# Optimization experiments

Hardware: AMD Instinct MI355X
Metric: run time of the kernel (lower is better)

## Reference

```python
import jax, jax.numpy as jnp
import numpy as np

N_NODES = 100000
N_EDGES = 600000
F_IN = 128
F_OUT = 128


def setup_inputs() -> dict:
    key = jax.random.key(0)
    ks = jax.random.split(key, 9)
    stdv = 1.0 / np.sqrt(F_OUT)
    return {
        "x": jax.random.normal(ks[0], (N_NODES, F_IN), dtype=jnp.float32),
        "weight": jax.random.uniform(ks[1], (F_IN, F_OUT), dtype=jnp.float32, minval=-stdv, maxval=stdv),
        "bias": jax.random.uniform(ks[2], (F_OUT,), dtype=jnp.float32, minval=-stdv, maxval=stdv),
        "vals0": jax.random.uniform(ks[3], (N_EDGES,), dtype=jnp.float32),
        "vals1": jax.random.uniform(ks[4], (N_EDGES,), dtype=jnp.float32),
        "rows0": jax.random.randint(ks[5], (N_EDGES,), 0, N_NODES, dtype=jnp.int32),
        "cols0": jax.random.randint(ks[6], (N_EDGES,), 0, N_NODES, dtype=jnp.int32),
        "rows1": jax.random.randint(ks[7], (N_EDGES,), 0, N_NODES, dtype=jnp.int32),
        "cols1": jax.random.randint(ks[8], (N_EDGES,), 0, N_NODES, dtype=jnp.int32),
    }


def _spmm(rows, cols, vals, dense, n):
    # COO sparse [n,n] @ dense [n,f]: gather source rows, scale, scatter-add to dest rows
    msgs = dense[cols] * vals[:, None]          # [E, f]
    return jax.ops.segment_sum(msgs, rows, num_segments=n)


def reference(x, weight, bias, vals0, vals1, rows0, cols0, rows1, cols1):
    n = x.shape[0]
    support = x @ weight                         # [N, F_OUT] dense GEMM
    out = _spmm(rows0, cols0, vals0, support, n) \
        + _spmm(rows1, cols1, vals1, support, n)
    return out + bias
```

## Files before the change

kernel.cpp:

```cpp
#include <hip/hip_runtime.h>


#define FDIM 128

typedef __attribute__((ext_vector_type(8))) short short8;
typedef __attribute__((ext_vector_type(4))) float floatx4;

__device__ __forceinline__ unsigned short f32_to_bf16(float f) {
    unsigned int u = __float_as_uint(f);
    unsigned int r = u + 0x7fffu + ((u >> 16) & 1u);
    return (unsigned short)(r >> 16);
}

__global__ __launch_bounds__(256) void wt_conv(const float* __restrict__ w,
                                               unsigned short* __restrict__ wt) {
    int idx = blockIdx.x * 256 + threadIdx.x;
    int nn = idx >> 7, k = idx & 127;
    wt[idx] = f32_to_bf16(w[(size_t)k * FDIM + nn]);
}

__global__ __launch_bounds__(256) void gemm_mfma(const float* __restrict__ x,
                                                 const unsigned short* __restrict__ wt,
                                                 unsigned short* __restrict__ support,
                                                 int n) {
    __shared__ __align__(16) short As[64][136];
    __shared__ __align__(16) short Bs[128][136];
    const int tid = threadIdx.x;
    const int m0 = blockIdx.x * 64;

    #pragma unroll
    for (int i = 0; i < 8; ++i) {
        int idx = tid + i * 256;
        int r = idx >> 5, c4 = idx & 31;
        float4 v = make_float4(0.f, 0.f, 0.f, 0.f);
        if (m0 + r < n) v = *(const float4*)(x + (size_t)(m0 + r) * FDIM + c4 * 4);
        short4 s;
        s.x = (short)f32_to_bf16(v.x); s.y = (short)f32_to_bf16(v.y);
        s.z = (short)f32_to_bf16(v.z); s.w = (short)f32_to_bf16(v.w);
        *(short4*)&As[r][c4 * 4] = s;
    }
    #pragma unroll
    for (int i = 0; i < 8; ++i) {
        int idx = tid + i * 256;
        int r = idx >> 4, c8 = idx & 15;
        short8 v = *(const short8*)(wt + (size_t)r * FDIM + c8 * 8);
        *(short8*)&Bs[r][c8 * 8] = v;
    }
    __syncthreads();

    const int wv = tid >> 6;
    const int lane = tid & 63;
    const int quad = lane >> 4;
    const int lr = lane & 15;

    floatx4 acc[8];
    #pragma unroll
    for (int nt = 0; nt < 8; ++nt) acc[nt] = (floatx4)0.f;

    #pragma unroll
    for (int ks = 0; ks < 4; ++ks) {
        short8 a = *(const short8*)&As[wv * 16 + lr][ks * 32 + quad * 8];
        #pragma unroll
        for (int nt = 0; nt < 8; ++nt) {
            short8 b = *(const short8*)&Bs[nt * 16 + lr][ks * 32 + quad * 8];
            acc[nt] = __builtin_amdgcn_mfma_f32_16x16x32_bf16(a, b, acc[nt], 0, 0, 0);
        }
    }

    #pragma unroll
    for (int i = 0; i < 4; ++i) {
        int row = m0 + wv * 16 + quad * 4 + i;
        if (row < n) {
            #pragma unroll
            for (int nt = 0; nt < 8; ++nt)
                support[(size_t)row * FDIM + nt * 16 + lr] = f32_to_bf16(acc[nt][i]);
        }
    }
}

__global__ __launch_bounds__(256) void build_rec(const int* __restrict__ rows0,
                                                 const int* __restrict__ cols0,
                                                 const float* __restrict__ vals0,
                                                 const int* __restrict__ rows1,
                                                 const int* __restrict__ cols1,
                                                 const float* __restrict__ vals1,
                                                 int* __restrict__ head,
                                                 int4* __restrict__ rec, int E) {
    int gid = blockIdx.x * 256 + threadIdx.x;
    if (gid >= 2 * E) return;
    int r, c; float v;
    if (gid < E) { r = rows0[gid]; c = cols0[gid]; v = vals0[gid]; }
    else         { int e = gid - E; r = rows1[e]; c = cols1[e]; v = vals1[e]; }
    int old = atomicExch(&head[r], gid);
    rec[gid] = make_int4(old, c, __float_as_int(v), 0);
}

__global__ __launch_bounds__(256) void pull_rec(const unsigned short* __restrict__ support,
                                                const int* __restrict__ head,
                                                const int4* __restrict__ rec,
                                                const float* __restrict__ bias,
                                                float* __restrict__ out, int n) {
    int wid = (blockIdx.x * 256 + threadIdx.x) >> 6;
    int lane = threadIdx.x & 63;
    if (wid >= n) return;
    float ax = 0.f, ay = 0.f;
    int e = head[wid];
    while (e >= 0) {
        int4 rc = rec[e];
        float v = __int_as_float(rc.z);
        unsigned int u = *(const unsigned int*)(support + (size_t)rc.y * FDIM + lane * 2);
        ax += v * __uint_as_float((u & 0xffffu) << 16);
        ay += v * __uint_as_float(u & 0xffff0000u);
        e = rc.x;
    }
    float2 b = *(const float2*)(bias + lane * 2);
    *(float2*)(out + (size_t)wid * FDIM + lane * 2) = make_float2(ax + b.x, ay + b.y);
}

__global__ __launch_bounds__(256) void init_bias(const float* __restrict__ bias,
                                                 float* __restrict__ out, int n) {
    int idx = blockIdx.x * 256 + threadIdx.x;
    int total = n * (FDIM / 4);
    if (idx < total) {
        int j = (idx & (FDIM / 4 - 1)) * 4;
        float4 b = *(const float4*)(bias + j);
        *(float4*)(out + (size_t)idx * 4) = b;
    }
}

__global__ __launch_bounds__(256) void scatter_bf16(
    const unsigned short* __restrict__ support,
    const int* __restrict__ rows0, const int* __restrict__ cols0, const float* __restrict__ vals0,
    const int* __restrict__ rows1, const int* __restrict__ cols1, const float* __restrict__ vals1,
    float* __restrict__ out, int E) {
    int gid = blockIdx.x * 256 + threadIdx.x;
    int lane = gid & 63;
    int eg = gid >> 6;
    if (eg >= 2 * E) return;
    int r, c; float v;
    if (eg < E) { r = rows0[eg]; c = cols0[eg]; v = vals0[eg]; }
    else        { int e = eg - E; r = rows1[e]; c = cols1[e]; v = vals1[e]; }
    unsigned int u = *(const unsigned int*)(support + (size_t)c * FDIM + lane * 2);
    float sx = __uint_as_float((u & 0xffffu) << 16);
    float sy = __uint_as_float(u & 0xffff0000u);
    float* op = out + (size_t)r * FDIM + lane * 2;
    atomicAdd(op,     sx * v);
    atomicAdd(op + 1, sy * v);
}

static inline size_t align256(size_t v) { return (v + 255) & ~(size_t)255; }

extern "C" void kernel_launch(void* const* d_in, const int* in_sizes, int n_in,
                              void* d_out, int out_size, void* d_ws, size_t ws_size,
                              hipStream_t stream) {
    const float* x     = (const float*)d_in[0];
    const float* w     = (const float*)d_in[1];
    const float* bias  = (const float*)d_in[2];
    const float* vals0 = (const float*)d_in[3];
    const float* vals1 = (const float*)d_in[4];
    const int*   rows0 = (const int*)d_in[5];
    const int*   cols0 = (const int*)d_in[6];
    const int*   rows1 = (const int*)d_in[7];
    const int*   cols1 = (const int*)d_in[8];
    const int n = in_sizes[0] / FDIM;
    const int E = in_sizes[3];
    float* out = (float*)d_out;

    size_t off = 0;
    unsigned short* support = (unsigned short*)((char*)d_ws + off);
    off = align256(off + (size_t)n * FDIM * 2);
    unsigned short* wt = (unsigned short*)((char*)d_ws + off);
    off = align256(off + (size_t)FDIM * FDIM * 2);
    int*  head = (int*)((char*)d_ws + off);   off = align256(off + (size_t)n * 4);
    int4* rec  = (int4*)((char*)d_ws + off);  off = align256(off + (size_t)2 * E * 16);

    wt_conv<<<(FDIM * FDIM) / 256, 256, 0, stream>>>(w, wt);
    gemm_mfma<<<(n + 63) / 64, 256, 0, stream>>>(x, wt, support, n);

    if (off <= ws_size) {
        hipMemsetAsync(head, 0xFF, (size_t)n * 4, stream);
        int eb = (2 * E + 255) / 256;
        build_rec<<<eb, 256, 0, stream>>>(rows0, cols0, vals0, rows1, cols1, vals1,
                                          head, rec, E);
        pull_rec<<<(n + 3) / 4, 256, 0, stream>>>(support, head, rec, bias, out, n);
    } else {
        int total4 = n * (FDIM / 4);
        init_bias<<<(total4 + 255) / 256, 256, 0, stream>>>(bias, out, n);
        long long tthreads = 2LL * E * 64;
        int blocks = (int)((tthreads + 255) / 256);
        scatter_bf16<<<blocks, 256, 0, stream>>>(support, rows0, cols0, vals0,
                                                 rows1, cols1, vals1, out, E);
    }
}
```

Baseline: 312.5 us.

## Convert linked-list edge records to CSR via scan and compact before pull

Adds per-row edge counts, a three-pass prefix scan to build row pointers, and a compaction kernel that walks each row's linked list into a contiguous CSR array. The pull kernel then loads up to 64 edges per wavefront cooperatively, broadcasts them with shuffles and issues two independent support gathers per iteration. This replaces the serial dependent pointer-chasing in the aggregation with parallel, coalesced index loads. The cost is extra kernels, an extra atomic per edge and a per-thread linked-list walk in compact.

```diff
diff --git a/kernel.cpp b/kernel.cpp
--- a/kernel.cpp
+++ b/kernel.cpp
@@ -2,6 +2,7 @@
 
 
 #define FDIM 128
+#define SCAN_TILE 2048
 
 typedef __attribute__((ext_vector_type(8))) short short8;
 typedef __attribute__((ext_vector_type(4))) float floatx4;
@@ -10,6 +11,12 @@
     unsigned int u = __float_as_uint(f);
     unsigned int r = u + 0x7fffu + ((u >> 16) & 1u);
     return (unsigned short)(r >> 16);
+}
+__device__ __forceinline__ float bf16_lo(unsigned int u) {
+    return __uint_as_float((u & 0xffffu) << 16);
+}
+__device__ __forceinline__ float bf16_hi(unsigned int u) {
+    return __uint_as_float(u & 0xffff0000u);
 }
 
 __global__ __launch_bounds__(256) void wt_conv(const float* __restrict__ w,
@@ -85,6 +92,7 @@
                                                  const int* __restrict__ cols1,
                                                  const float* __restrict__ vals1,
                                                  int* __restrict__ head,
+                                                 int* __restrict__ counts,
                                                  int4* __restrict__ rec, int E) {
     int gid = blockIdx.x * 256 + threadIdx.x;
     if (gid >= 2 * E) return;
@@ -92,26 +100,128 @@
     if (gid < E) { r = rows0[gid]; c = cols0[gid]; v = vals0[gid]; }
     else         { int e = gid - E; r = rows1[e]; c = cols1[e]; v = vals1[e]; }
     int old = atomicExch(&head[r], gid);
+    atomicAdd(&counts[r], 1);
     rec[gid] = make_int4(old, c, __float_as_int(v), 0);
 }
 
-__global__ __launch_bounds__(256) void pull_rec(const unsigned short* __restrict__ support,
-                                                const int* __restrict__ head,
-                                                const int4* __restrict__ rec,
+__global__ __launch_bounds__(256) void scan_p1(const int* __restrict__ counts,
+                                               int* __restrict__ blockSums, int n) {
+    __shared__ int sdata[256];
+    const int t = threadIdx.x;
+    const int base = blockIdx.x * SCAN_TILE + t * 8;
+    int sum = 0;
+    #pragma unroll
+    for (int i = 0; i < 8; ++i) {
+        int idx = base + i;
+        if (idx < n) sum += counts[idx];
+    }
+    sdata[t] = sum;
+    __syncthreads();
+    for (int d = 128; d > 0; d >>= 1) {
+        if (t < d) sdata[t] += sdata[t + d];
+        __syncthreads();
+    }
+    if (t == 0) blockSums[blockIdx.x] = sdata[0];
+}
+
+__global__ __launch_bounds__(512) void scan_p2(int* __restrict__ blockSums,
+                                               int* __restrict__ rowptr,
+                                               int nb, int n) {
+    __shared__ int sdata[512];
+    const int t = threadIdx.x;
+    int v = (t < nb) ? blockSums[t] : 0;
+    sdata[t] = v;
+    __syncthreads();
+    for (int d = 1; d < 512; d <<= 1) {
+        int u = (t >= d) ? sdata[t - d] : 0;
+        __syncthreads();
+        sdata[t] += u;
+        __syncthreads();
+    }
+    if (t < nb) blockSums[t] = sdata[t] - v;
+    if (t == 511) rowptr[n] = sdata[511];
+}
+
+__global__ __launch_bounds__(256) void scan_p3(const int* __restrict__ counts,
+                                               const int* __restrict__ blockSums,
+                                               int* __restrict__ rowptr, int n) {
+    __shared__ int sdata[256];
+    const int t = threadIdx.x;
+    const int base = blockIdx.x * SCAN_TILE + t * 8;
+    int loc[8];
+    int sum = 0;
+    #pragma unroll
+    for (int i = 0; i < 8; ++i) {
+        int idx = base + i;
+        int c = (idx < n) ? counts[idx] : 0;
+        loc[i] = sum;
+        sum += c;
+    }
+    sdata[t] = sum;
+    __syncthreads();
+    const int mine = sum;
+    for (int d = 1; d < 256; d <<= 1) {
+        int u = (t >= d) ? sdata[t - d] : 0;
+        __syncthreads();
+        sdata[t] += u;
+        __syncthreads();
+    }
+    const int off = sdata[t] - mine + blockSums[blockIdx.x];
+    #pragma unroll
+    for (int i = 0; i < 8; ++i) {
+        int idx = base + i;
+        if (idx < n) rowptr[idx] = off + loc[i];
+    }
+}
+
+__global__ __launch_bounds__(256) void compact(const int* __restrict__ head,
+                                               const int4* __restrict__ rec,
+                                               const int* __restrict__ rowptr,
+                                               int2* __restrict__ csr, int n) {
+    int r = blockIdx.x * 256 + threadIdx.x;
+    if (r >= n) return;
+    int pos = rowptr[r];
+    int e = head[r];
+    while (e >= 0) {
+        int4 rc = rec[e];
+        csr[pos++] = make_int2(rc.y, rc.z);
+        e = rc.x;
+    }
+}
+
+__global__ __launch_bounds__(256) void pull_csr(const unsigned short* __restrict__ support,
+                                                const int* __restrict__ rowptr,
+                                                const int2* __restrict__ csr,
                                                 const float* __restrict__ bias,
                                                 float* __restrict__ out, int n) {
     int wid = (blockIdx.x * 256 + threadIdx.x) >> 6;
     int lane = threadIdx.x & 63;
     if (wid >= n) return;
+    int s = rowptr[wid];
+    int e = rowptr[wid + 1];
     float ax = 0.f, ay = 0.f;
-    int e = head[wid];
-    while (e >= 0) {
-        int4 rc = rec[e];
-        float v = __int_as_float(rc.z);
-        unsigned int u = *(const unsigned int*)(support + (size_t)rc.y * FDIM + lane * 2);
-        ax += v * __uint_as_float((u & 0xffffu) << 16);
-        ay += v * __uint_as_float(u & 0xffff0000u);
-        e = rc.x;
+    for (int base = s; base < e; base += 64) {
+        int len = min(64, e - base);
+        int2 me = make_int2(0, 0);
+        if (lane < len) me = csr[base + lane];
+        int j = 0;
+        for (; j + 1 < len; j += 2) {
+            int   c0 = __shfl(me.x, j);
+            int   c1 = __shfl(me.x, j + 1);
+            float v0 = __int_as_float(__shfl(me.y, j));
+            float v1 = __int_as_float(__shfl(me.y, j + 1));
+            unsigned int u0 = *(const unsigned int*)(support + (size_t)c0 * FDIM + lane * 2);
+            unsigned int u1 = *(const unsigned int*)(support + (size_t)c1 * FDIM + lane * 2);
+            ax += v0 * bf16_lo(u0) + v1 * bf16_lo(u1);
+            ay += v0 * bf16_hi(u0) + v1 * bf16_hi(u1);
+        }
+        if (j < len) {
+            int   c = __shfl(me.x, j);
+            float v = __int_as_float(__shfl(me.y, j));
+            unsigned int u = *(const unsigned int*)(support + (size_t)c * FDIM + lane * 2);
+            ax += v * bf16_lo(u);
+            ay += v * bf16_hi(u);
+        }
     }
     float2 b = *(const float2*)(bias + lane * 2);
     *(float2*)(out + (size_t)wid * FDIM + lane * 2) = make_float2(ax + b.x, ay + b.y);
@@ -141,11 +251,9 @@
     if (eg < E) { r = rows0[eg]; c = cols0[eg]; v = vals0[eg]; }
     else        { int e = eg - E; r = rows1[e]; c = cols1[e]; v = vals1[e]; }
     unsigned int u = *(const unsigned int*)(support + (size_t)c * FDIM + lane * 2);
-    float sx = __uint_as_float((u & 0xffffu) << 16);
-    float sy = __uint_as_float(u & 0xffff0000u);
     float* op = out + (size_t)r * FDIM + lane * 2;
-    atomicAdd(op,     sx * v);
-    atomicAdd(op + 1, sy * v);
+    atomicAdd(op,     bf16_lo(u) * v);
+    atomicAdd(op + 1, bf16_hi(u) * v);
 }
 
 static inline size_t align256(size_t v) { return (v + 255) & ~(size_t)255; }
@@ -166,23 +274,34 @@
     const int E = in_sizes[3];
     float* out = (float*)d_out;
 
+    const int nScanBlocks = (n + SCAN_TILE - 1) / SCAN_TILE;
+
     size_t off = 0;
     unsigned short* support = (unsigned short*)((char*)d_ws + off);
     off = align256(off + (size_t)n * FDIM * 2);
     unsigned short* wt = (unsigned short*)((char*)d_ws + off);
     off = align256(off + (size_t)FDIM * FDIM * 2);
-    int*  head = (int*)((char*)d_ws + off);   off = align256(off + (size_t)n * 4);
-    int4* rec  = (int4*)((char*)d_ws + off);  off = align256(off + (size_t)2 * E * 16);
+    int*  head      = (int*)((char*)d_ws + off);  off = align256(off + (size_t)n * 4);
+    int*  counts    = (int*)((char*)d_ws + off);  off = align256(off + (size_t)n * 4);
+    int*  rowptr    = (int*)((char*)d_ws + off);  off = align256(off + (size_t)(n + 1) * 4);
+    int*  blockSums = (int*)((char*)d_ws + off);  off = align256(off + (size_t)nScanBlocks * 4);
+    int4* rec       = (int4*)((char*)d_ws + off); off = align256(off + (size_t)2 * E * 16);
+    int2* csr       = (int2*)((char*)d_ws + off); off = align256(off + (size_t)2 * E * 8);
 
     wt_conv<<<(FDIM * FDIM) / 256, 256, 0, stream>>>(w, wt);
     gemm_mfma<<<(n + 63) / 64, 256, 0, stream>>>(x, wt, support, n);
 
-    if (off <= ws_size) {
+    if (off <= ws_size && nScanBlocks <= 512) {
         hipMemsetAsync(head, 0xFF, (size_t)n * 4, stream);
+        hipMemsetAsync(counts, 0, (size_t)n * 4, stream);
         int eb = (2 * E + 255) / 256;
         build_rec<<<eb, 256, 0, stream>>>(rows0, cols0, vals0, rows1, cols1, vals1,
-                                          head, rec, E);
-        pull_rec<<<(n + 3) / 4, 256, 0, stream>>>(support, head, rec, bias, out, n);
+                                          head, counts, rec, E);
+        scan_p1<<<nScanBlocks, 256, 0, stream>>>(counts, blockSums, n);
+        scan_p2<<<1, 512, 0, stream>>>(blockSums, rowptr, nScanBlocks, n);
+        scan_p3<<<nScanBlocks, 256, 0, stream>>>(counts, blockSums, rowptr, n);
+        compact<<<(n + 255) / 256, 256, 0, stream>>>(head, rec, rowptr, csr, n);
+        pull_csr<<<(n + 3) / 4, 256, 0, stream>>>(support, rowptr, csr, bias, out, n);
     } else {
         int total4 = n * (FDIM / 4);
         init_bias<<<(total4 + 255) / 256, 256, 0, stream>>>(bias, out, n);
```

Result: slower. 339.7 us (+8.7%).
